# Kernel optimization log

Hardware: AMD Instinct MI355X
Metric: run time of the kernel (lower is better)

Reference implementation:

```python
import jax, jax.numpy as jnp
import numpy as np

B, T, D_LAT = 128, 256, 256
N_HIDDEN = 1024
H_SMALL = N_HIDDEN // 2  # 512: lstm1/lstm2 hidden size
H_BIG = N_HIDDEN         # 1024: lstm3 hidden size


def _p(key, shape, scale=0.05):
    return (jax.random.normal(key, shape, dtype=jnp.float32) * scale)


def setup_inputs() -> dict:
    key = jax.random.key(0)
    ks = jax.random.split(key, 16)
    return {
        "X": jax.random.normal(ks[0], (B, T, D_LAT), dtype=jnp.float32),
        # LSTMCell 1: input D_LAT -> hidden H_SMALL (torch layout: [4H, in])
        "W_ih1": _p(ks[1], (4 * H_SMALL, D_LAT)),
        "W_hh1": _p(ks[2], (4 * H_SMALL, H_SMALL)),
        "b_ih1": _p(ks[3], (4 * H_SMALL,)),
        "b_hh1": _p(ks[4], (4 * H_SMALL,)),
        # LSTMCell 2: H_SMALL -> H_SMALL
        "W_ih2": _p(ks[5], (4 * H_SMALL, H_SMALL)),
        "W_hh2": _p(ks[6], (4 * H_SMALL, H_SMALL)),
        "b_ih2": _p(ks[7], (4 * H_SMALL,)),
        "b_hh2": _p(ks[8], (4 * H_SMALL,)),
        # LSTMCell 3: H_SMALL -> H_BIG
        "W_ih3": _p(ks[9], (4 * H_BIG, H_SMALL)),
        "W_hh3": _p(ks[10], (4 * H_BIG, H_BIG)),
        "b_ih3": _p(ks[11], (4 * H_BIG,)),
        "b_hh3": _p(ks[12], (4 * H_BIG,)),
        # Linear: H_BIG -> D_LAT (torch layout: [out, in])
        "W_lin": _p(ks[13], (D_LAT, H_BIG)),
        "b_lin": _p(ks[14], (D_LAT,)),
    }


def _lstm_cell(x, h, c, W_ih, W_hh, b_ih, b_hh):
    # torch.nn.LSTMCell gate order: i, f, g, o
    gates = x @ W_ih.T + b_ih + h @ W_hh.T + b_hh  # [B, 4H]
    i, f, g, o = jnp.split(gates, 4, axis=-1)
    c_new = jax.nn.sigmoid(f) * c + jax.nn.sigmoid(i) * jnp.tanh(g)
    h_new = jax.nn.sigmoid(o) * jnp.tanh(c_new)
    return h_new, c_new


def reference(X, W_ih1, W_hh1, b_ih1, b_hh1,
              W_ih2, W_hh2, b_ih2, b_hh2,
              W_ih3, W_hh3, b_ih3, b_hh3,
              W_lin, b_lin):
    n = X.shape[0]
    z_s = jnp.zeros((n, H_SMALL), dtype=X.dtype)
    z_b = jnp.zeros((n, H_BIG), dtype=X.dtype)
    init = (z_s, z_s, z_s, z_s, z_b, z_b)

    def step(carry, x_t):
        h1, c1, h2, c2, h3, c3 = carry
        h1, c1 = _lstm_cell(x_t, h1, c1, W_ih1, W_hh1, b_ih1, b_hh1)
        h2, c2 = _lstm_cell(h1, h2, c2, W_ih2, W_hh2, b_ih2, b_hh2)
        h3, c3 = _lstm_cell(h2, h3, c3, W_ih3, W_hh3, b_ih3, b_hh3)
        out = h3 @ W_lin.T + b_lin  # [B, D_LAT]
        return (h1, c1, h2, c2, h3, c3), out

    xs = jnp.swapaxes(X, 0, 1)  # [T, B, D_LAT]
    _, outputs = jax.lax.scan(step, init, xs)
    return outputs  # [T, B, D_LAT] == torch.stack(outputs) with future=0
```

## Files before the change

kernel.cpp:

```cpp
#include <hip/hip_runtime.h>
#include <stdint.h>

#define NWG 208

typedef __attribute__((ext_vector_type(8))) short short8;
typedef __attribute__((ext_vector_type(4))) float floatx4;
typedef __attribute__((ext_vector_type(4))) unsigned int uintx4;

static constexpr int Bb = 128, Tt = 256, Dl = 256, Hs = 512, Hb = 1024;
static constexpr int D = 32;

static constexpr size_t OFF_FLAGS = 0;
static constexpr size_t OFF_B1  = 1024;
static constexpr size_t OFF_B2  = OFF_B1 + 2048*4;
static constexpr size_t OFF_B3  = OFF_B2 + 2048*4;
static constexpr size_t OFF_BL  = OFF_B3 + 4096*4;
static constexpr size_t OFF_W1  = OFF_BL + 1024;
static constexpr size_t OFF_W2  = OFF_W1 + (size_t)2048*768*2;
static constexpr size_t OFF_W3  = OFF_W2 + (size_t)2048*1024*2;
static constexpr size_t OFF_WL  = OFF_W3 + (size_t)4096*1536*2;
static constexpr size_t FIXED_END = OFF_WL + (size_t)256*1024*2;
static constexpr size_t OFF_H1R  = FIXED_END;
static constexpr size_t OFF_H2R  = OFF_H1R + (size_t)D*Bb*Hs*2;
static constexpr size_t OFF_H3R  = OFF_H2R + (size_t)D*Bb*Hs*2;
static constexpr size_t OFF_XALL = OFF_H3R + (size_t)D*Bb*Hb*2;
static constexpr size_t WS_NEED  = OFF_XALL + (size_t)Tt*Bb*Dl*2;

static constexpr int SMEM_BYTES = 135168;
static constexpr int STG_OFF    = 131072;

__device__ __forceinline__ unsigned short f2bf(float f) {
  unsigned int u = __float_as_uint(f);
  unsigned int r = (u + 0x7fffu + ((u >> 16) & 1u)) >> 16;
  return (unsigned short)r;
}
__device__ __forceinline__ float sigm(float x) { return 1.f/(1.f + __expf(-x)); }
__device__ __forceinline__ float tanh_f(float x) {
  x = fminf(fmaxf(x, -15.f), 15.f);
  float e = __expf(-2.f*x);
  return (1.f - e)/(1.f + e);
}
__device__ __forceinline__ size_t blk_off(int row, int u) {
  return ((size_t)(u >> 5)*8 + (row >> 4))*512 + (size_t)((u & 31) >> 3)*128
       + (size_t)(row & 15)*8 + (u & 7);
}
__device__ __forceinline__ void st_dword_cg(void* p, unsigned int v) {
  asm volatile("global_store_dword %0, %1, off sc0 sc1" :: "v"(p), "v"(v) : "memory");
}
__device__ __forceinline__ void st_b128_cg(void* p, uintx4 v) {
  asm volatile("global_store_dwordx4 %0, %1, off sc0 sc1" :: "v"(p), "v"(v) : "memory");
}
__device__ __forceinline__ void waitcnt_vm0() {
  asm volatile("s_waitcnt vmcnt(0)" ::: "memory");
}

__device__ __forceinline__ void wait_ge(const unsigned int* f, int n, int tgt, int lane) {
  if (tgt <= 0) return;
  for (;;) {
    int ok = 1;
    for (int i = lane; i < n; i += 64) {
      unsigned v;
      asm volatile("global_load_dword %0, %1, off sc0 sc1\n\ts_waitcnt vmcnt(0)"
                   : "=v"(v) : "v"(f + i) : "memory");
      if ((int)v < tgt) ok = 0;
    }
    if (__all(ok)) return;
    __builtin_amdgcn_s_sleep(2);
  }
}

__global__ void lstm_init(
    const float* __restrict__ X,
    const float* __restrict__ Wih1, const float* __restrict__ Whh1,
    const float* __restrict__ bih1, const float* __restrict__ bhh1,
    const float* __restrict__ Wih2, const float* __restrict__ Whh2,
    const float* __restrict__ bih2, const float* __restrict__ bhh2,
    const float* __restrict__ Wih3, const float* __restrict__ Whh3,
    const float* __restrict__ bih3, const float* __restrict__ bhh3,
    const float* __restrict__ Wlin, const float* __restrict__ blin,
    unsigned char* __restrict__ ws)
{
  size_t i0 = (size_t)blockIdx.x*blockDim.x + threadIdx.x;
  size_t np = (size_t)gridDim.x*blockDim.x;

  unsigned int* fl = (unsigned int*)(ws + OFF_FLAGS);
  for (size_t i = i0; i < 256; i += np) fl[i] = 0u;

  float* b1 = (float*)(ws + OFF_B1);
  float* b2 = (float*)(ws + OFF_B2);
  float* b3 = (float*)(ws + OFF_B3);
  float* bl = (float*)(ws + OFF_BL);
  for (size_t i = i0; i < 2048; i += np) b1[i] = bih1[i] + bhh1[i];
  for (size_t i = i0; i < 2048; i += np) b2[i] = bih2[i] + bhh2[i];
  for (size_t i = i0; i < 4096; i += np) b3[i] = bih3[i] + bhh3[i];
  for (size_t i = i0; i < 256;  i += np) bl[i] = blin[i];

  unsigned short* w1 = (unsigned short*)(ws + OFF_W1);
  unsigned short* w2 = (unsigned short*)(ws + OFF_W2);
  unsigned short* w3 = (unsigned short*)(ws + OFF_W3);
  unsigned short* wl = (unsigned short*)(ws + OFF_WL);
  for (size_t i = i0; i < (size_t)2048*768; i += np) {
    size_t r = i/768, k = i - r*768;
    float v = (k < 256) ? Wih1[r*256 + k] : Whh1[r*512 + (k - 256)];
    w1[i] = f2bf(v);
  }
  for (size_t i = i0; i < (size_t)2048*1024; i += np) {
    size_t r = i >> 10, k = i & 1023;
    float v = (k < 512) ? Wih2[r*512 + k] : Whh2[r*512 + (k - 512)];
    w2[i] = f2bf(v);
  }
  for (size_t i = i0; i < (size_t)4096*1536; i += np) {
    size_t r = i/1536, k = i - r*1536;
    float v = (k < 512) ? Wih3[r*512 + k] : Whh3[r*1024 + (k - 512)];
    w3[i] = f2bf(v);
  }
  for (size_t i = i0; i < (size_t)256*1024; i += np) wl[i] = f2bf(Wlin[i]);

  unsigned short* rings = (unsigned short*)(ws + OFF_H1R);
  const size_t nring = (size_t)D*Bb*Hs + (size_t)D*Bb*Hs + (size_t)D*Bb*Hb;
  for (size_t i = i0; i < nring; i += np) rings[i] = 0;

  unsigned short* xall = (unsigned short*)(ws + OFF_XALL);
  for (size_t i = i0; i < (size_t)Tt*Bb*Dl; i += np) {
    size_t t = i >> 15, rem = i & 32767;
    size_t b = rem >> 8, d = rem & 255;
    xall[t*32768 + blk_off((int)b, (int)d)] = f2bf(X[(b*(size_t)Tt + t)*Dl + d]);
  }
}

template<int TYPE>
__device__ __forceinline__ void layer_phase(
    const unsigned short* __restrict__ segA,
    const unsigned short* __restrict__ segB,
    unsigned short* __restrict__ hout,
    unsigned char* __restrict__ smem,
    const float* __restrict__ bias_r,
    float (&creg)[2][2][4],
    int U0, int wv, int lane, int tid)
{
  constexpr int K    = (TYPE==0 ? 768 : TYPE==1 ? 1024 : 1536);
  constexpr int KB1  = (TYPE==0 ? 256 : 512);
  constexpr int MF   = (TYPE==2 ? 1 : 2);
  constexpr int CKS  = (TYPE==2 ? 8 : 4);
  constexpr int NCH  = K/(32*CKS);
  const int l15 = lane & 15;
  const int g   = l15 >> 2;
  const int mbase = (TYPE==2 ? wv*16 : (wv&3)*32);
  const int nfb   = (TYPE==2 ? 0 : (wv>>2)*2);

  const size_t lof = (size_t)(lane >> 4)*128 + (size_t)l15*8;
  const unsigned short* pa[MF];
  const unsigned short* pb[MF];
  #pragma unroll
  for (int mf = 0; mf < MF; ++mf) {
    const size_t rb = (size_t)((mbase >> 4) + mf)*512;
    pa[mf] = segA + rb + lof;
    pb[mf] = segB + rb + lof;
  }
  int rowbyte[2], xr[2];
  #pragma unroll
  for (int nf = 0; nf < 2; ++nf) {
    const int rp = (nfb + nf)*16 + l15;
    rowbyte[nf] = rp*(K*2);
    xr[nf] = (rp & 7) << 4;
  }
  const int klobyte = ((lane >> 4) << 3)*2;

  floatx4 acc[MF][2];
  #pragma unroll
  for (int mf = 0; mf < MF; ++mf)
    #pragma unroll
    for (int nf = 0; nf < 2; ++nf) {
      float bv = bias_r[nf];
      floatx4 b4 = {bv, bv, bv, bv};
      acc[mf][nf] = b4;
    }

  short8 A0[CKS][MF], A1[CKS][MF];
  auto LOADC = [&](int c, short8 (&A)[CKS][MF]) {
    #pragma unroll
    for (int ks = 0; ks < CKS; ++ks) {
      const int kb = (c*CKS + ks)*32;
      #pragma unroll
      for (int mf = 0; mf < MF; ++mf) {
        const unsigned short* p = (kb < KB1)
            ? pa[mf] + (size_t)(kb >> 5)*4096
            : pb[mf] + (size_t)((kb - KB1) >> 5)*4096;
        A[ks][mf] = *(const short8*)p;
      }
    }
  };
  auto MM = [&](int c, short8 (&A)[CKS][MF]) {
    #pragma unroll
    for (int ks = 0; ks < CKS; ++ks) {
      const int kb = (c*CKS + ks)*32;
      short8 bf[2];
      #pragma unroll
      for (int nf = 0; nf < 2; ++nf)
        bf[nf] = *(const short8*)(smem + rowbyte[nf] + ((kb*2 + klobyte) ^ xr[nf]));
      #pragma unroll
      for (int mf = 0; mf < MF; ++mf)
        #pragma unroll
        for (int nf = 0; nf < 2; ++nf)
          acc[mf][nf] = __builtin_amdgcn_mfma_f32_16x16x32_bf16(A[ks][mf], bf[nf], acc[mf][nf], 0, 0, 0);
    }
  };

  LOADC(0, A0);
  #pragma unroll 1
  for (int ch = 0; ch < NCH; ch += 2) {
    LOADC(ch + 1, A1);
    MM(ch, A0);
    if (ch + 2 < NCH) LOADC(ch + 2, A0);
    MM(ch + 1, A1);
  }

  unsigned short* stg = (unsigned short*)(smem + STG_OFF);
  const int a = (U0 & 31) >> 3;
  #pragma unroll
  for (int nf = 0; nf < 2; ++nf) {
    const int u = U0 + (nfb + nf)*4 + (l15 & 3);
    #pragma unroll
    for (int mf = 0; mf < MF; ++mf) {
      float h4[4];
      #pragma unroll
      for (int j = 0; j < 4; ++j) {
        float s0  = acc[mf][nf][j];
        float s4  = __shfl_xor(s0, 4);
        float s8  = __shfl_xor(s0, 8);
        float s12 = __shfl_xor(s0, 12);
        float iv = (g==0)?s0 :(g==1)?s4 :(g==2)?s8 :s12;
        float fv = (g==0)?s4 :(g==1)?s0 :(g==2)?s12:s8;
        float gv = (g==0)?s8 :(g==1)?s12:(g==2)?s0 :s4;
        float ov = (g==0)?s12:(g==1)?s8 :(g==2)?s4 :s0;
        float c  = sigm(fv)*creg[mf][nf][j] + sigm(iv)*tanh_f(gv);
        creg[mf][nf][j] = c;
        h4[j] = sigm(ov)*tanh_f(c);
      }
      float hs = (g==0)?h4[0]:(g==1)?h4[1]:(g==2)?h4[2]:h4[3];
      const int row = mbase + mf*16 + ((lane >> 4) << 2) + g;
      const int c2  = (TYPE==2) ? (row >> 4)
                                : ((row >> 4)*2 + (((u & 31) >> 3) - a));
      stg[c2*128 + (row & 15)*8 + (u & 7)] = f2bf(hs);
    }
  }
  __syncthreads();

  const size_t gbase = (size_t)(U0 >> 5)*4096;
  if (TYPE == 2) {
    if (tid < 128) {
      const int c2 = tid >> 4, w = tid & 15;
      short8 v = *(const short8*)(stg + c2*128 + w*8);
      st_b128_cg(hout + gbase + (size_t)c2*512 + (size_t)a*128 + w*8, *(uintx4*)&v);
    }
  } else {
    if (tid < 256) {
      const int c2 = tid >> 4, w = tid & 15;
      short8 v = *(const short8*)(stg + c2*128 + w*8);
      st_b128_cg(hout + gbase + (size_t)(c2 >> 1)*512 + (size_t)(a + (c2 & 1))*128 + w*8, *(uintx4*)&v);
    }
  }
}

__global__ void __launch_bounds__(512, 2)
lstm_persist(float* __restrict__ out, unsigned char* __restrict__ ws)
{
  extern __shared__ unsigned char smem[];

  __builtin_amdgcn_fence(__ATOMIC_ACQUIRE, "agent");

  const int tid  = threadIdx.x;
  const int lane = tid & 63;
  const int wv   = tid >> 6;
  const int wg   = blockIdx.x;
  const int l15  = lane & 15;

  unsigned int* flags = (unsigned int*)(ws + OFF_FLAGS);
  const float* bias1 = (const float*)(ws + OFF_B1);
  const float* bias2 = (const float*)(ws + OFF_B2);
  const float* bias3 = (const float*)(ws + OFF_B3);
  const float* biasl = (const float*)(ws + OFF_BL);
  const unsigned short* W1 = (const unsigned short*)(ws + OFF_W1);
  const unsigned short* W2 = (const unsigned short*)(ws + OFF_W2);
  const unsigned short* W3 = (const unsigned short*)(ws + OFF_W3);
  const unsigned short* WL = (const unsigned short*)(ws + OFF_WL);
  unsigned short* h1r = (unsigned short*)(ws + OFF_H1R);
  unsigned short* h2r = (unsigned short*)(ws + OFF_H2R);
  unsigned short* h3r = (unsigned short*)(ws + OFF_H3R);
  unsigned short* Xall = (unsigned short*)(ws + OFF_XALL);

  auto slot = [](int t) -> size_t { return (size_t)(t & (D - 1)); };
  const size_t HSs = (size_t)Bb*Hs, HBs = (size_t)Bb*Hb, XBs = (size_t)Bb*Dl;

  int type, U0 = 0, osec = 0, K = 0, WROWS = 0, HGATE = 0;
  const unsigned short* Wg = nullptr; const float* biasp = nullptr;
  if (wg < 32)        { type = 0; U0 = wg*16;        Wg = W1; biasp = bias1; K = 768;  WROWS = 64; HGATE = 512; }
  else if (wg < 64)   { type = 1; U0 = (wg-32)*16;   Wg = W2; biasp = bias2; K = 1024; WROWS = 64; HGATE = 512; }
  else if (wg < 192)  { type = 2; U0 = (wg-64)*8;    Wg = W3; biasp = bias3; K = 1536; WROWS = 32; HGATE = 1024; }
  else                { type = 3; osec = (wg-192)*16; Wg = WL; K = 1024; WROWS = 16; }

  {
    const int rowchunks = K >> 3;
    for (int idx = tid; idx < WROWS*rowchunks; idx += 512) {
      const int rp = idx / rowchunks, kc = idx - rp*rowchunks;
      int R;
      if (type == 3) R = osec + rp;
      else {
        const int c = rp & 15;
        R = (c >> 2)*HGATE + U0 + (rp >> 4)*4 + (c & 3);
      }
      uintx4 v = *(const uintx4*)(Wg + (size_t)R*K + kc*8);
      const int db = rp*(K*2) + ((kc*16) ^ ((rp & 7) << 4));
      *(uintx4*)(smem + db) = v;
    }
  }

  float bias_r[2] = {0.f, 0.f};
  if (type < 3) {
    const int g   = l15 >> 2;
    const int nfb = (type == 2 ? 0 : (wv >> 2)*2);
    #pragma unroll
    for (int nf = 0; nf < 2; ++nf) {
      const int u = U0 + (nfb + nf)*4 + (l15 & 3);
      bias_r[nf] = biasp[g*HGATE + u];
    }
  } else {
    bias_r[0] = biasl[osec + l15];
  }

  float creg[2][2][4];
  #pragma unroll
  for (int a = 0; a < 2; ++a)
    #pragma unroll
    for (int b = 0; b < 2; ++b)
      #pragma unroll
      for (int c = 0; c < 4; ++c) creg[a][b][c] = 0.f;

  __syncthreads();

  for (int t = 0; t < Tt; ++t) {
    if (wv == 0) {
      if (type == 0)      { wait_ge(flags + 0, 32, t, lane);
                            wait_ge(flags + 32, 32, t - 31, lane); }
      else if (type == 1) { wait_ge(flags + 0, 32, t + 1, lane);
                            wait_ge(flags + 32, 32, t, lane);
                            wait_ge(flags + 64, 128, t - 31, lane); }
      else if (type == 2) { wait_ge(flags + 32, 32, t + 1, lane);
                            wait_ge(flags + 64, 128, t, lane);
                            wait_ge(flags + 192, 16, t - 31, lane); }
      else                { wait_ge(flags + 64, 128, t + 1, lane); }
    }
    __syncthreads();

    if (type == 0) {
      layer_phase<0>(Xall + (size_t)t*XBs,
                     h1r + slot(t-1)*HSs,
                     h1r + slot(t)*HSs,
                     smem, bias_r, creg, U0, wv, lane, tid);
    } else if (type == 1) {
      layer_phase<1>(h1r + slot(t)*HSs,
                     h2r + slot(t-1)*HSs,
                     h2r + slot(t)*HSs,
                     smem, bias_r, creg, U0, wv, lane, tid);
    } else if (type == 2) {
      layer_phase<2>(h2r + slot(t)*HSs,
                     h3r + slot(t-1)*HBs,
                     h3r + slot(t)*HBs,
                     smem, bias_r, creg, U0, wv, lane, tid);
    } else {
      const unsigned short* hA = h3r + slot(t)*HBs;
      const size_t lof = (size_t)(lane >> 4)*128 + (size_t)l15*8;
      const unsigned short* pa0 = hA + (size_t)wv*512 + lof;
      const int rowbyte = l15*2048;
      const int xr = (l15 & 7) << 4;
      const int klobyte = ((lane >> 4) << 3)*2;
      floatx4 oacc;
      { floatx4 b4 = {bias_r[0], bias_r[0], bias_r[0], bias_r[0]}; oacc = b4; }
      short8 A0[4], A1[4];
      auto HLOAD = [&](int c, short8 (&A)[4]) {
        #pragma unroll
        for (int ks = 0; ks < 4; ++ks)
          A[ks] = *(const short8*)(pa0 + (size_t)(c*4 + ks)*4096);
      };
      auto HMM = [&](int c, short8 (&A)[4]) {
        #pragma unroll
        for (int ks = 0; ks < 4; ++ks) {
          const int kb = c*128 + ks*32;
          short8 bw = *(const short8*)(smem + rowbyte + ((kb*2 + klobyte) ^ xr));
          oacc = __builtin_amdgcn_mfma_f32_16x16x32_bf16(A[ks], bw, oacc, 0, 0, 0);
        }
      };
      HLOAD(0, A0);
      #pragma unroll 1
      for (int ch = 0; ch < 8; ch += 2) {
        HLOAD(ch + 1, A1);
        HMM(ch, A0);
        if (ch + 2 < 8) HLOAD(ch + 2, A0);
        HMM(ch + 1, A1);
      }
      const int col = osec + l15;
      const int b0 = wv*16 + ((lane >> 4) << 2);
      #pragma unroll
      for (int j = 0; j < 4; ++j)
        st_dword_cg(out + ((size_t)t*Bb + b0 + j)*Dl + col,
                    __float_as_uint(oacc[j]));
    }

    waitcnt_vm0();
    __syncthreads();
    if (tid == 0) st_dword_cg(flags + wg, (unsigned)(t + 1));
    if ((t & 7) == 7)
      __builtin_amdgcn_fence(__ATOMIC_ACQUIRE, "agent");
  }
}

extern "C" void kernel_launch(void* const* d_in, const int* in_sizes, int n_in,
                              void* d_out, int out_size, void* d_ws, size_t ws_size,
                              hipStream_t stream)
{
  if (ws_size < WS_NEED) return;

  const float* X    = (const float*)d_in[0];
  const float* Wih1 = (const float*)d_in[1];
  const float* Whh1 = (const float*)d_in[2];
  const float* bih1 = (const float*)d_in[3];
  const float* bhh1 = (const float*)d_in[4];
  const float* Wih2 = (const float*)d_in[5];
  const float* Whh2 = (const float*)d_in[6];
  const float* bih2 = (const float*)d_in[7];
  const float* bhh2 = (const float*)d_in[8];
  const float* Wih3 = (const float*)d_in[9];
  const float* Whh3 = (const float*)d_in[10];
  const float* bih3 = (const float*)d_in[11];
  const float* bhh3 = (const float*)d_in[12];
  const float* Wlin = (const float*)d_in[13];
  const float* blin = (const float*)d_in[14];
  unsigned char* ws = (unsigned char*)d_ws;

  lstm_init<<<2048, 256, 0, stream>>>(X, Wih1, Whh1, bih1, bhh1,
                                      Wih2, Whh2, bih2, bhh2,
                                      Wih3, Whh3, bih3, bhh3,
                                      Wlin, blin, ws);
  lstm_persist<<<NWG, 512, SMEM_BYTES, stream>>>((float*)d_out, ws);
}
```

Before: 3.470 ms.

## Parallelize flag polling across waves and triple-buffer weight fragment loads

Flag polling now reads four flags per lane with one dwordx4 load. Each dependency wait is given to its own wave rather than run one after another on wave 0. The slot-reuse backpressure lag shrinks from 31 steps to a fixed LAG of 4. The GEMM inner loop moves from a double-buffered loop that is not unrolled to a fully unrolled triple-buffered prefetch of A fragments. The aim is lower per-step synchronization latency and more memory-latency hiding, at the cost of more registers and code size, and a tighter producer-consumer coupling that may stall producers more often.

```diff
diff --git a/kernel.cpp b/kernel.cpp
--- a/kernel.cpp
+++ b/kernel.cpp
@@ -9,6 +9,7 @@
 
 static constexpr int Bb = 128, Tt = 256, Dl = 256, Hs = 512, Hb = 1024;
 static constexpr int D = 32;
+static constexpr int LAG = 4;
 
 static constexpr size_t OFF_FLAGS = 0;
 static constexpr size_t OFF_B1  = 1024;
@@ -56,13 +57,14 @@
 
 __device__ __forceinline__ void wait_ge(const unsigned int* f, int n, int tgt, int lane) {
   if (tgt <= 0) return;
+  const int nl = n >> 2;
   for (;;) {
     int ok = 1;
-    for (int i = lane; i < n; i += 64) {
-      unsigned v;
-      asm volatile("global_load_dword %0, %1, off sc0 sc1\n\ts_waitcnt vmcnt(0)"
-                   : "=v"(v) : "v"(f + i) : "memory");
-      if ((int)v < tgt) ok = 0;
+    if (lane < nl) {
+      uintx4 v;
+      asm volatile("global_load_dwordx4 %0, %1, off sc0 sc1\n\ts_waitcnt vmcnt(0)"
+                   : "=v"(v) : "v"(f + lane*4) : "memory");
+      if ((int)v[0] < tgt || (int)v[1] < tgt || (int)v[2] < tgt || (int)v[3] < tgt) ok = 0;
     }
     if (__all(ok)) return;
     __builtin_amdgcn_s_sleep(2);
@@ -176,7 +178,7 @@
       acc[mf][nf] = b4;
     }
 
-  short8 A0[CKS][MF], A1[CKS][MF];
+  short8 B0[CKS][MF], B1[CKS][MF], B2[CKS][MF];
   auto LOADC = [&](int c, short8 (&A)[CKS][MF]) {
     #pragma unroll
     for (int ks = 0; ks < CKS; ++ks) {
@@ -205,14 +207,14 @@
           acc[mf][nf] = __builtin_amdgcn_mfma_f32_16x16x32_bf16(A[ks][mf], bf[nf], acc[mf][nf], 0, 0, 0);
     }
   };
-
-  LOADC(0, A0);
-  #pragma unroll 1
-  for (int ch = 0; ch < NCH; ch += 2) {
-    LOADC(ch + 1, A1);
-    MM(ch, A0);
-    if (ch + 2 < NCH) LOADC(ch + 2, A0);
-    MM(ch + 1, A1);
+  auto LOADB = [&](int c, int b) { if (b == 0) LOADC(c, B0); else if (b == 1) LOADC(c, B1); else LOADC(c, B2); };
+  auto MMB   = [&](int c, int b) { if (b == 0) MM(c, B0);    else if (b == 1) MM(c, B1);    else MM(c, B2); };
+
+  LOADB(0, 0); LOADB(1, 1); LOADB(2, 2);
+  #pragma unroll
+  for (int ch = 0; ch < NCH; ++ch) {
+    MMB(ch, ch % 3);
+    if (ch + 3 < NCH) LOADB(ch + 3, ch % 3);
   }
 
   unsigned short* stg = (unsigned short*)(smem + STG_OFF);
@@ -339,16 +341,19 @@
   __syncthreads();
 
   for (int t = 0; t < Tt; ++t) {
-    if (wv == 0) {
-      if (type == 0)      { wait_ge(flags + 0, 32, t, lane);
-                            wait_ge(flags + 32, 32, t - 31, lane); }
-      else if (type == 1) { wait_ge(flags + 0, 32, t + 1, lane);
-                            wait_ge(flags + 32, 32, t, lane);
-                            wait_ge(flags + 64, 128, t - 31, lane); }
-      else if (type == 2) { wait_ge(flags + 32, 32, t + 1, lane);
-                            wait_ge(flags + 64, 128, t, lane);
-                            wait_ge(flags + 192, 16, t - 31, lane); }
-      else                { wait_ge(flags + 64, 128, t + 1, lane); }
+    if (type == 0) {
+      if (wv == 0)      wait_ge(flags + 0, 32, t, lane);
+      else if (wv == 1) wait_ge(flags + 32, 32, t - LAG, lane);
+    } else if (type == 1) {
+      if (wv == 0)      wait_ge(flags + 0, 32, t + 1, lane);
+      else if (wv == 1) wait_ge(flags + 32, 32, t, lane);
+      else if (wv == 2) wait_ge(flags + 64, 128, t - LAG, lane);
+    } else if (type == 2) {
+      if (wv == 0)      wait_ge(flags + 32, 32, t + 1, lane);
+      else if (wv == 1) wait_ge(flags + 64, 128, t, lane);
+      else if (wv == 2) wait_ge(flags + 192, 16, t - LAG, lane);
+    } else {
+      if (wv == 0)      wait_ge(flags + 64, 128, t + 1, lane);
     }
     __syncthreads();
 
```

Result: faster. 3.381 ms, median of 2 (-2.6%).
